# Kernel tuning notes

Hardware: AMD Instinct MI355X
Metric: run time of the kernel (lower is better)

Reference implementation:

```python
import jax, jax.numpy as jnp
import numpy as np

B, T, C, H = 2, 2048, 1024, 16
D = C // H  # head dim = 64


def setup_inputs() -> dict:
    key = jax.random.key(0)
    ks = jax.random.split(key, 5)
    s = 0.02
    return {
        "x": jax.random.normal(ks[0], (B, T, C), dtype=jnp.float32),
        "W_attn": jax.random.normal(ks[1], (C, 3 * C), dtype=jnp.float32) * s,
        "b_attn": jax.random.normal(ks[2], (3 * C,), dtype=jnp.float32) * s,
        "W_proj": jax.random.normal(ks[3], (C, C), dtype=jnp.float32) * s,
        "b_proj": jax.random.normal(ks[4], (C,), dtype=jnp.float32) * s,
    }


def reference(x, W_attn, b_attn, W_proj, b_proj):
    Bb, Tt, Cc = x.shape
    kqv = x @ W_attn + b_attn                     # [B,T,3C]
    q, k, v = jnp.split(kqv, 3, axis=2)           # each [B,T,C]
    # reshape to heads: [B,H,T,D]
    q = q.reshape(Bb, Tt, H, D).transpose(0, 2, 1, 3)
    k = k.reshape(Bb, Tt, H, D).transpose(0, 2, 1, 3)
    v = v.reshape(Bb, Tt, H, D).transpose(0, 2, 1, 3)
    scale = 1.0 / jnp.sqrt(jnp.float32(D))
    att = jnp.einsum('bhqd,bhkd->bhqk', q, k) * scale  # [B,H,T,T]
    causal = jnp.tril(jnp.ones((Tt, Tt), dtype=bool))
    att = jnp.where(causal[None, None], att, -jnp.inf)
    att = jax.nn.softmax(att, axis=-1)
    y = jnp.einsum('bhqk,bhkd->bhqd', att, v)      # [B,H,T,D]
    y = y.transpose(0, 2, 1, 3).reshape(Bb, Tt, Cc)
    return y @ W_proj + b_proj
```

## Files before the change

### kernel.cpp

```cpp
#include <hip/hip_runtime.h>
#include <hip/hip_bf16.h>
#include <math.h>

typedef __attribute__((ext_vector_type(4))) float f32x4;
typedef __attribute__((ext_vector_type(8))) short short8;
typedef __attribute__((ext_vector_type(4))) short short4v;

__device__ __forceinline__ short f2bf(float f) {
    union { __hip_bfloat16 h; short s; } u;
    u.h = __float2bfloat16(f);
    return u.s;
}

__device__ __forceinline__ float bf2f(short s) {
    union { float f; unsigned u; } x;
    x.u = ((unsigned)(unsigned short)s) << 16;
    return x.f;
}

__device__ __forceinline__ f32x4 mfma16(short8 a, short8 b, f32x4 c) {
    return __builtin_amdgcn_mfma_f32_16x16x32_bf16(a, b, c, 0, 0, 0);
}

__global__ __launch_bounds__(256) void cvt_bf16(const float* __restrict__ in,
                                                short* __restrict__ out, int n) {
    int i = (blockIdx.x * 256 + threadIdx.x) * 8;
    if (i >= n) return;
    float4 a = *reinterpret_cast<const float4*>(in + i);
    float4 b = *reinterpret_cast<const float4*>(in + i + 4);
    short8 o;
    o[0] = f2bf(a.x); o[1] = f2bf(a.y); o[2] = f2bf(a.z); o[3] = f2bf(a.w);
    o[4] = f2bf(b.x); o[5] = f2bf(b.y); o[6] = f2bf(b.z); o[7] = f2bf(b.w);
    *reinterpret_cast<short8*>(out + i) = o;
}

__global__ __launch_bounds__(256) void transpose_w(const float* __restrict__ W,
                                                   short* __restrict__ Wt,
                                                   int K, int N) {
    __shared__ float tile[64][68];
    const int k0 = blockIdx.x * 64;
    const int n0 = blockIdx.y * 64;
    const int tid = threadIdx.x;
    #pragma unroll
    for (int i = 0; i < 4; ++i) {
        int c = tid + i * 256;
        int r = c >> 4;
        int col4 = (c & 15) * 4;
        float4 v = *reinterpret_cast<const float4*>(W + (size_t)(k0 + r) * N + n0 + col4);
        tile[r][col4 + 0] = v.x; tile[r][col4 + 1] = v.y;
        tile[r][col4 + 2] = v.z; tile[r][col4 + 3] = v.w;
    }
    __syncthreads();
    #pragma unroll
    for (int i = 0; i < 4; ++i) {
        int c = tid + i * 256;
        int r2 = c >> 4;
        int col4 = (c & 15) * 4;
        short4v o;
        #pragma unroll
        for (int j = 0; j < 4; ++j) o[j] = f2bf(tile[col4 + j][r2]);
        *reinterpret_cast<short4v*>(Wt + (size_t)(n0 + r2) * K + k0 + col4) = o;
    }
}

template<int MODE>
__global__ __launch_bounds__(256) void gemm_bt(const short* __restrict__ A,
                                               const short* __restrict__ Bt,
                                               const float* __restrict__ bias,
                                               void* __restrict__ C,
                                               short* __restrict__ vt,
                                               int M, int N, int K) {
    constexpr int BM = 128, BN = 128, BK = 64, LDP = BK + 8;
    __shared__ short As[BM * LDP];
    __shared__ short Bs[BN * LDP];
    const int tid = threadIdx.x;
    const int lane = tid & 63, wave = tid >> 6;
    const int bm = blockIdx.x * BM, bn = blockIdx.y * BN;
    const int wr = (wave >> 1) * 64, wc = (wave & 1) * 64;
    const int g = lane >> 4, l15 = lane & 15;

    f32x4 acc[4][4] = {};

    for (int k0 = 0; k0 < K; k0 += BK) {
        __syncthreads();
        #pragma unroll
        for (int i = 0; i < 4; ++i) {
            int c = tid + i * 256;
            int r = c >> 3;
            int col = (c & 7) * 8;
            *reinterpret_cast<short8*>(&As[r * LDP + col]) =
                *reinterpret_cast<const short8*>(A + (size_t)(bm + r) * K + k0 + col);
            *reinterpret_cast<short8*>(&Bs[r * LDP + col]) =
                *reinterpret_cast<const short8*>(Bt + (size_t)(bn + r) * K + k0 + col);
        }
        __syncthreads();
        #pragma unroll
        for (int kk = 0; kk < 2; ++kk) {
            short8 af[4], bfr[4];
            #pragma unroll
            for (int m = 0; m < 4; ++m)
                af[m] = *reinterpret_cast<const short8*>(&As[(wr + m * 16 + l15) * LDP + kk * 32 + g * 8]);
            #pragma unroll
            for (int n = 0; n < 4; ++n)
                bfr[n] = *reinterpret_cast<const short8*>(&Bs[(wc + n * 16 + l15) * LDP + kk * 32 + g * 8]);
            #pragma unroll
            for (int m = 0; m < 4; ++m)
                #pragma unroll
                for (int n = 0; n < 4; ++n)
                    acc[m][n] = mfma16(af[m], bfr[n], acc[m][n]);
        }
    }

    #pragma unroll
    for (int m = 0; m < 4; ++m)
        #pragma unroll
        for (int n = 0; n < 4; ++n) {
            int gc = bn + wc + n * 16 + l15;
            float bv = bias[gc];
            int gr0 = bm + wr + m * 16 + g * 4;
            if (MODE == 0) {
                #pragma unroll
                for (int r = 0; r < 4; ++r)
                    reinterpret_cast<float*>(C)[(size_t)(gr0 + r) * N + gc] = acc[m][n][r] + bv;
            } else {
                if (gc < 2048) {
                    float sc = (gc < 1024) ? 0.125f : 1.0f;
                    short* qkp = reinterpret_cast<short*>(C);
                    #pragma unroll
                    for (int r = 0; r < 4; ++r)
                        qkp[(size_t)(gr0 + r) * 2048 + gc] = f2bf((acc[m][n][r] + bv) * sc);
                } else {
                    int cv = gc - 2048;
                    int bb = gr0 >> 11;
                    int t0 = gr0 & 2047;
                    short4v o;
                    #pragma unroll
                    for (int r = 0; r < 4; ++r) o[r] = f2bf(acc[m][n][r] + bv);
                    *reinterpret_cast<short4v*>(&vt[((size_t)(bb << 10) + cv) * 2048 + t0]) = o;
                }
            }
        }
}


template<int NMAX, int KKMAX, bool MASK>
__device__ __forceinline__ void tile_step(const short* __restrict__ Kl,
                                          const short* __restrict__ Vl,
                                          short* Ps, int l15, int g,
                                          const short8 (&qf)[2][2],
                                          f32x4 (&oacc)[2][4],
                                          f32x4 (&lacc)[2],
                                          float (&mst)[2][4],
                                          int rowbase, int colbase,
                                          short8 ones) {
    f32x4 sacc[2][NMAX + 1];
    #pragma unroll
    for (int m = 0; m < 2; ++m)
        #pragma unroll
        for (int n = 0; n <= NMAX; ++n) sacc[m][n] = f32x4{0.f, 0.f, 0.f, 0.f};
    __builtin_amdgcn_s_setprio(1);
    #pragma unroll
    for (int kk = 0; kk < 2; ++kk)
        #pragma unroll
        for (int n = 0; n <= NMAX; ++n) {
            short8 kf = *reinterpret_cast<const short8*>(Kl + (size_t)n * 16 * 2048 + kk * 32);
            sacc[0][n] = mfma16(qf[0][kk], kf, sacc[0][n]);
            sacc[1][n] = mfma16(qf[1][kk], kf, sacc[1][n]);
        }
    __builtin_amdgcn_s_setprio(0);

    short8 vf[KKMAX + 1][4];
    #pragma unroll
    for (int kk = 0; kk <= KKMAX; ++kk)
        #pragma unroll
        for (int nd = 0; nd < 4; ++nd)
            vf[kk][nd] = *reinterpret_cast<const short8*>(Vl + (size_t)nd * 16 * 2048 + kk * 32);

    if (MASK) {
        #pragma unroll
        for (int m = 0; m < 2; ++m)
            #pragma unroll
            for (int n = 0; n <= NMAX; ++n)
                #pragma unroll
                for (int r = 0; r < 4; ++r) {
                    int row = rowbase + m * 16 + r;
                    int col = colbase + n * 16;
                    if (col > row) sacc[m][n][r] = -INFINITY;
                }
    }

    #pragma unroll
    for (int m = 0; m < 2; ++m)
        #pragma unroll
        for (int r = 0; r < 4; ++r) {
            float rm = sacc[m][0][r];
            #pragma unroll
            for (int n = 1; n <= NMAX; ++n) rm = fmaxf(rm, sacc[m][n][r]);
            #pragma unroll
            for (int w = 1; w < 16; w <<= 1) rm = fmaxf(rm, __shfl_xor(rm, w));
            float mn = fmaxf(mst[m][r], rm);
            float corr = __expf(mst[m][r] - mn);
            mst[m][r] = mn;
            #pragma unroll
            for (int n = 0; n <= NMAX; ++n) {
                float p = __expf(sacc[m][n][r] - mn);
                Ps[(g * 4 + m * 16 + r) * 72 + n * 16 + l15] = f2bf(p);
            }
            lacc[m][r] *= corr;
            #pragma unroll
            for (int nd = 0; nd < 4; ++nd) oacc[m][nd][r] *= corr;
        }

    __builtin_amdgcn_s_setprio(1);
    #pragma unroll
    for (int kk = 0; kk <= KKMAX; ++kk) {
        short8 pa0 = *reinterpret_cast<const short8*>(&Ps[l15 * 72 + kk * 32 + g * 8]);
        short8 pa1 = *reinterpret_cast<const short8*>(&Ps[(16 + l15) * 72 + kk * 32 + g * 8]);
        #pragma unroll
        for (int nd = 0; nd < 4; ++nd) {
            oacc[0][nd] = mfma16(pa0, vf[kk][nd], oacc[0][nd]);
            oacc[1][nd] = mfma16(pa1, vf[kk][nd], oacc[1][nd]);
        }
        lacc[0] = mfma16(pa0, ones, lacc[0]);
        lacc[1] = mfma16(pa1, ones, lacc[1]);
    }
    __builtin_amdgcn_s_setprio(0);
}

__global__ __launch_bounds__(64) void attn_chunk(const short* __restrict__ qk,
                                                 const short* __restrict__ vt,
                                                 short* __restrict__ yatt,
                                                 short* __restrict__ part) {
    constexpr int T = 2048;
    __shared__ short Ps[32 * 72];

    const int lane = threadIdx.x & 63;
    const int g = lane >> 4, l15 = lane & 15;

    const int bid = blockIdx.x;
    const int xcd = bid & 7;
    const int idx = bid >> 3;
    const int g4 = idx / 120;
    const int c = 119 - (idx - g4 * 120);
    const int grp = xcd * 4 + g4;
    const int h = grp & 15, b = grp >> 4;
    int qt, ch;
    if (c < 24)      { qt = c; ch = 0; }
    else if (c < 72) { int t = c - 24; qt = 24 + (t >> 1); ch = t & 1; }
    else             { int t = c - 72; int q3 = t / 3; qt = 48 + q3; ch = t - q3 * 3; }

    const int nsteps = (qt >> 1) + 1;
    const int s0 = ch * 12;
    const int s1 = (s0 + 12 < nsteps) ? s0 + 12 : nsteps;
    const bool hasdiag = (s1 == nsteps);
    const int nfull = s1 - s0 - (hasdiag ? 1 : 0);

    const int qs = qt * 32;
    const size_t baseQ = (size_t)b * T * 2048 + (size_t)h * 64;
    const short* Kl = qk + baseQ + 1024 + (size_t)l15 * 2048 + g * 8;
    const short* Vl = vt + ((size_t)b * 1024 + (size_t)h * 64) * 2048 + (size_t)l15 * 2048 + g * 8;

    short8 ones;
    #pragma unroll
    for (int i = 0; i < 8; ++i) ones[i] = (short)0x3F80;

    short8 qf[2][2];
    #pragma unroll
    for (int m = 0; m < 2; ++m)
        #pragma unroll
        for (int kk = 0; kk < 2; ++kk)
            qf[m][kk] = *reinterpret_cast<const short8*>(
                qk + baseQ + (size_t)(qs + m * 16 + l15) * 2048 + kk * 32 + g * 8);

    f32x4 oacc[2][4] = {};
    f32x4 lacc[2] = {};
    float mst[2][4];
    #pragma unroll
    for (int m = 0; m < 2; ++m)
        #pragma unroll
        for (int r = 0; r < 4; ++r) mst[m][r] = -INFINITY;

    const int rowbase = qs + g * 4;
    int colbase = l15 + s0 * 64;
    const short* Klj = Kl + (size_t)s0 * 64 * 2048;
    const short* Vlj = Vl + s0 * 64;

    for (int j = 0; j < nfull; ++j) {
        tile_step<3, 1, false>(Klj, Vlj, Ps, l15, g, qf, oacc, lacc, mst, rowbase, colbase, ones);
        Klj += 64 * 2048;
        Vlj += 64;
        colbase += 64;
    }
    if (hasdiag) {
        if (qt & 1)
            tile_step<3, 1, true>(Klj, Vlj, Ps, l15, g, qf, oacc, lacc, mst, rowbase, colbase, ones);
        else
            tile_step<1, 0, true>(Klj, Vlj, Ps, l15, g, qf, oacc, lacc, mst, rowbase, colbase, ones);
    }

    if (qt < 24) {
        #pragma unroll
        for (int m = 0; m < 2; ++m)
            #pragma unroll
            for (int r = 0; r < 4; ++r) {
                float rl = 1.0f / lacc[m][r];
                int row = qs + m * 16 + g * 4 + r;
                #pragma unroll
                for (int nd = 0; nd < 4; ++nd) {
                    int col = nd * 16 + l15;
                    yatt[((size_t)b * T + row) * 1024 + h * 64 + col] = f2bf(oacc[m][nd][r] * rl);
                }
            }
    } else {
        const int p = grp * 96 + ((qt < 48) ? (qt - 24) * 2 + ch : 48 + (qt - 48) * 3 + ch);
        short* Pp = part + (size_t)p * 2112;
        #pragma unroll
        for (int m = 0; m < 2; ++m)
            #pragma unroll
            for (int r = 0; r < 4; ++r) {
                float rl = 1.0f / lacc[m][r];
                int rloc = m * 16 + g * 4 + r;
                #pragma unroll
                for (int nd = 0; nd < 4; ++nd)
                    Pp[rloc * 64 + nd * 16 + l15] = f2bf(oacc[m][nd][r] * rl);
            }
        if (l15 == 0) {
            float* Lp = reinterpret_cast<float*>(Pp + 2048);
            #pragma unroll
            for (int m = 0; m < 2; ++m)
                #pragma unroll
                for (int r = 0; r < 4; ++r)
                    Lp[m * 16 + g * 4 + r] = mst[m][r] + __logf(lacc[m][r]);
        }
    }
}

__global__ __launch_bounds__(64) void attn_merge(const short* __restrict__ part,
                                                 short* __restrict__ yatt) {
    const int bid = blockIdx.x;
    const int xcd = bid & 7;
    const int idx = bid >> 3;
    const int g4 = idx / 40;
    const int qt = 24 + (idx - g4 * 40);
    const int grp = xcd * 4 + g4;
    const int h = grp & 15, b = grp >> 4;
    const int nc = (qt < 48) ? 2 : 3;
    const int p0 = grp * 96 + ((qt < 48) ? (qt - 24) * 2 : 48 + (qt - 48) * 3);
    const int d = threadIdx.x & 63;

    const short* P0 = part + (size_t)p0 * 2112;
    #pragma unroll 4
    for (int r = 0; r < 32; ++r) {
        float lse[3], mx;
        lse[0] = reinterpret_cast<const float*>(P0 + 2048)[r];
        lse[1] = reinterpret_cast<const float*>(P0 + 2112 + 2048)[r];
        mx = fmaxf(lse[0], lse[1]);
        if (nc == 3) {
            lse[2] = reinterpret_cast<const float*>(P0 + 2 * 2112 + 2048)[r];
            mx = fmaxf(mx, lse[2]);
        }
        float w0 = __expf(lse[0] - mx);
        float w1 = __expf(lse[1] - mx);
        float wsum = w0 + w1;
        float acc = w0 * bf2f(P0[r * 64 + d]) + w1 * bf2f(P0[2112 + r * 64 + d]);
        if (nc == 3) {
            float w2 = __expf(lse[2] - mx);
            wsum += w2;
            acc += w2 * bf2f(P0[2 * 2112 + r * 64 + d]);
        }
        yatt[((size_t)b * 2048 + qt * 32 + r) * 1024 + h * 64 + d] = f2bf(acc / wsum);
    }
}

extern "C" void kernel_launch(void* const* d_in, const int* in_sizes, int n_in,
                              void* d_out, int out_size, void* d_ws, size_t ws_size,
                              hipStream_t stream) {
    constexpr int B = 2, T = 2048, C = 1024;
    constexpr int M = B * T;
    constexpr int N1 = 3 * C;
    constexpr int K = C;

    const float* x      = (const float*)d_in[0];
    const float* W_attn = (const float*)d_in[1];
    const float* b_attn = (const float*)d_in[2];
    const float* W_proj = (const float*)d_in[3];
    const float* b_proj = (const float*)d_in[4];
    float* out = (float*)d_out;

    char* ws = (char*)d_ws;
    short* x_bf    = (short*)(ws);
    short* Wt_attn = (short*)(ws + 8388608);
    short* Wt_proj = (short*)(ws + 14680064);
    short* qk      = (short*)(ws + 16777216);
    short* vt      = (short*)(ws + 33554432);
    short* yatt    = (short*)(ws + 41943040);
    short* part    = (short*)(ws);

    cvt_bf16<<<dim3(M * K / (256 * 8)), 256, 0, stream>>>(x, x_bf, M * K);
    transpose_w<<<dim3(K / 64, N1 / 64), 256, 0, stream>>>(W_attn, Wt_attn, K, N1);
    transpose_w<<<dim3(K / 64, C / 64), 256, 0, stream>>>(W_proj, Wt_proj, K, C);

    gemm_bt<1><<<dim3(M / 128, N1 / 128), 256, 0, stream>>>(x_bf, Wt_attn, b_attn, qk, vt, M, N1, K);
    attn_chunk<<<dim3(3840), 64, 0, stream>>>(qk, vt, yatt, part);
    attn_merge<<<dim3(1280), 64, 0, stream>>>(part, yatt);
    gemm_bt<0><<<dim3(M / 128, C / 128), 256, 0, stream>>>(yatt, Wt_proj, b_proj, out, nullptr, M, C, C);
}
```

Before: 192.4 us.

## Pack four attention waves per block and skip rescale unless max grows

The attention kernel now launches 256-thread blocks that each hold four independent single-wave work items, each with its own shared P buffer, instead of one wave per block. The goal is to cut block-launch and scheduling overhead and to let waves from neighbouring q-tiles share cache. Separately, the online-softmax rescale of the output and sum accumulators now runs only when some row's new maximum exceeds the stored maximum by more than 8. This is a lazy rescaling trick that saves exp and multiply work but lets exponentials grow up to about e^8 before a rescale. It also adds a wave-wide branch.

New measurement: 194.4 us. No clear change (+1.0%).

```diff
diff --git a/kernel.cpp b/kernel.cpp
--- a/kernel.cpp
+++ b/kernel.cpp
@@ -189,26 +189,48 @@
                 }
     }
 
+    float rm[2][4];
     #pragma unroll
     for (int m = 0; m < 2; ++m)
         #pragma unroll
         for (int r = 0; r < 4; ++r) {
-            float rm = sacc[m][0][r];
-            #pragma unroll
-            for (int n = 1; n <= NMAX; ++n) rm = fmaxf(rm, sacc[m][n][r]);
-            #pragma unroll
-            for (int w = 1; w < 16; w <<= 1) rm = fmaxf(rm, __shfl_xor(rm, w));
-            float mn = fmaxf(mst[m][r], rm);
-            float corr = __expf(mst[m][r] - mn);
-            mst[m][r] = mn;
+            float v = sacc[m][0][r];
+            #pragma unroll
+            for (int n = 1; n <= NMAX; ++n) v = fmaxf(v, sacc[m][n][r]);
+            #pragma unroll
+            for (int w = 1; w < 16; w <<= 1) v = fmaxf(v, __shfl_xor(v, w));
+            rm[m][r] = v;
+        }
+
+    bool grow = false;
+    #pragma unroll
+    for (int m = 0; m < 2; ++m)
+        #pragma unroll
+        for (int r = 0; r < 4; ++r)
+            grow = grow || (rm[m][r] > mst[m][r] + 8.0f);
+    if (__any(grow)) {
+        #pragma unroll
+        for (int m = 0; m < 2; ++m)
+            #pragma unroll
+            for (int r = 0; r < 4; ++r) {
+                float mn = fmaxf(mst[m][r], rm[m][r]);
+                float corr = __expf(mst[m][r] - mn);
+                mst[m][r] = mn;
+                lacc[m][r] *= corr;
+                #pragma unroll
+                for (int nd = 0; nd < 4; ++nd) oacc[m][nd][r] *= corr;
+            }
+    }
+
+    #pragma unroll
+    for (int m = 0; m < 2; ++m)
+        #pragma unroll
+        for (int r = 0; r < 4; ++r) {
             #pragma unroll
             for (int n = 0; n <= NMAX; ++n) {
-                float p = __expf(sacc[m][n][r] - mn);
+                float p = __expf(sacc[m][n][r] - mst[m][r]);
                 Ps[(g * 4 + m * 16 + r) * 72 + n * 16 + l15] = f2bf(p);
             }
-            lacc[m][r] *= corr;
-            #pragma unroll
-            for (int nd = 0; nd < 4; ++nd) oacc[m][nd][r] *= corr;
         }
 
     __builtin_amdgcn_s_setprio(1);
@@ -227,21 +249,24 @@
     __builtin_amdgcn_s_setprio(0);
 }
 
-__global__ __launch_bounds__(64) void attn_chunk(const short* __restrict__ qk,
-                                                 const short* __restrict__ vt,
-                                                 short* __restrict__ yatt,
-                                                 short* __restrict__ part) {
+__global__ __launch_bounds__(256) void attn_chunk(const short* __restrict__ qk,
+                                                  const short* __restrict__ vt,
+                                                  short* __restrict__ yatt,
+                                                  short* __restrict__ part) {
     constexpr int T = 2048;
-    __shared__ short Ps[32 * 72];
-
-    const int lane = threadIdx.x & 63;
+    __shared__ short PsAll[4][32 * 72];
+
+    const int tid = threadIdx.x;
+    const int wave = tid >> 6, lane = tid & 63;
     const int g = lane >> 4, l15 = lane & 15;
+    short* Ps = PsAll[wave];
 
     const int bid = blockIdx.x;
     const int xcd = bid & 7;
     const int idx = bid >> 3;
-    const int g4 = idx / 120;
-    const int c = 119 - (idx - g4 * 120);
+    const int g4 = idx / 30;
+    const int q = idx - g4 * 30;
+    const int c = 119 - (q * 4 + wave);
     const int grp = xcd * 4 + g4;
     const int h = grp & 15, b = grp >> 4;
     int qt, ch;
@@ -401,7 +426,7 @@
     transpose_w<<<dim3(K / 64, C / 64), 256, 0, stream>>>(W_proj, Wt_proj, K, C);
 
     gemm_bt<1><<<dim3(M / 128, N1 / 128), 256, 0, stream>>>(x_bf, Wt_attn, b_attn, qk, vt, M, N1, K);
-    attn_chunk<<<dim3(3840), 64, 0, stream>>>(qk, vt, yatt, part);
+    attn_chunk<<<dim3(960), 256, 0, stream>>>(qk, vt, yatt, part);
     attn_merge<<<dim3(1280), 64, 0, stream>>>(part, yatt);
     gemm_bt<0><<<dim3(M / 128, C / 128), 256, 0, stream>>>(yatt, Wt_proj, b_proj, out, nullptr, M, C, C);
 }
```
